# Performance work log

Hardware: AMD Instinct MI355X
Metric: run time of the kernel (lower is better)

The kernel has to match this reference:

```python
import jax, jax.numpy as jnp
import numpy as np

N_VOCAB = 50000
V_SUPPORT = 20000
D = 300
H = 512
B = 8192


def setup_inputs() -> dict:
    key = jax.random.key(0)
    ks = jax.random.split(key, 8)
    ws = jax.random.randint(ks[0], (B,), 0, N_VOCAB, dtype=jnp.int64 if jax.config.jax_enable_x64 else jnp.int32)
    cs = jax.random.randint(ks[1], (B,), 0, N_VOCAB, dtype=ws.dtype)
    vectors = jax.random.normal(ks[2], (N_VOCAB, D), dtype=jnp.float32)
    W1 = jax.random.normal(ks[3], (D, H), dtype=jnp.float32) * (1.0 / np.sqrt(D))
    b1 = jnp.zeros((H,), dtype=jnp.float32)
    W2 = jax.random.normal(ks[4], (H, V_SUPPORT), dtype=jnp.float32) * (1.0 / np.sqrt(H))
    b2 = jnp.zeros((V_SUPPORT,), dtype=jnp.float32)
    vector_to_support = jax.random.randint(ks[5], (N_VOCAB,), 0, V_SUPPORT, dtype=ws.dtype)
    return {"ws": ws, "cs": cs, "vectors": vectors, "W1": W1, "b1": b1,
            "W2": W2, "b2": b2, "vector_to_support": vector_to_support}


def reference(ws, cs, vectors, W1, b1, W2, b2, vector_to_support):
    # embedding lookup of context vectors: [B, D]
    v_c = vectors[cs]
    # FeedForward: Linear -> ReLU -> Linear, then LogSoftmax over support
    h = jax.nn.relu(v_c @ W1 + b1)            # [B, H]
    logits = h @ W2 + b2                       # [B, V]
    logp = jax.nn.log_softmax(logits, axis=-1) # [B, V]
    # map target word (vocab index) -> support index, gather per-row logprob.
    # Original does outputs.T[idx].diag() (O(B^2)); the fused equivalent is a
    # per-row gather: logp[arange(B), idx].
    w_sup = vector_to_support[ws]              # [B]
    logprobs = jnp.take_along_axis(logp, w_sup[:, None], axis=-1)[:, 0]
    return -logprobs                            # [B] NLL per example
```

## Files before the change

kernel.cpp:

```cpp
#include <hip/hip_runtime.h>
#include <hip/hip_bf16.h>
#include <hip/hip_fp8.h>
#include <math.h>


typedef __bf16 bf16x8 __attribute__((ext_vector_type(8)));
typedef float f32x4 __attribute__((ext_vector_type(4)));
typedef int i32x4 __attribute__((ext_vector_type(4)));
typedef int i32x8 __attribute__((ext_vector_type(8)));

#define B_N 8192
#define D_N 300
#define K1K 320
#define H_N 512
#define V_N 20000
#define V_PAD 20480
#define NSPLIT 16
#define SPLIT_V 1280
#define NCH 40
#define ROWS_BLK 128
#define CHUNK_BYTES 16384

#define OFF_PART (8388608u)
#define OFF_W1T  (OFF_PART + 16u*8192u*8u)
#define OFF_B2L  (OFF_W1T + 512u*320u*2u)
#define OFF_H8   (OFF_B2L + 20480u*4u)
#define OFF_W2T8 (OFF_H8 + 8192u*512u)

#define SCALE1 0x7F7F7F7F
#define LOG2E  1.4426950408889634f

__device__ inline unsigned short f2bf(float f) {
  __hip_bfloat16 h = __float2bfloat16(f);
  return *reinterpret_cast<unsigned short*>(&h);
}

__device__ inline unsigned char f2fp8(float f) {
  __hip_fp8_e4m3 q(f);
  return (unsigned char)q.__x;
}

__device__ inline unsigned int pk4_fp8(float a, float b, float c, float d) {
#if __has_builtin(__builtin_amdgcn_cvt_pk_fp8_f32)
  int v = 0;
  v = __builtin_amdgcn_cvt_pk_fp8_f32(a, b, v, false);
  v = __builtin_amdgcn_cvt_pk_fp8_f32(c, d, v, true);
  return (unsigned int)v;
#else
  return (unsigned int)f2fp8(a) | ((unsigned int)f2fp8(b) << 8) |
         ((unsigned int)f2fp8(c) << 16) | ((unsigned int)f2fp8(d) << 24);
#endif
}

__device__ inline float fp82f(unsigned char b) {
  __hip_fp8_e4m3 q; q.__x = b;
  return (float)q;
}

__device__ __forceinline__ void gl16(const void* g, void* l) {
  __builtin_amdgcn_global_load_lds(
      (const __attribute__((address_space(1))) void*)g,
      (__attribute__((address_space(3))) void*)l, 16, 0, 0);
}

__global__ __launch_bounds__(256) void kprep_a(
    const float* __restrict__ W1, unsigned int* __restrict__ W1Tu,
    const float* __restrict__ b2, float* __restrict__ b2l)
{
  __shared__ float tile[64][65];
  const int bid = blockIdx.x;
  const int tid = threadIdx.x;
  if (bid < 40) {
    const int n0 = (bid & 7) * 64;
    const int k0 = (bid >> 3) * 64;
    #pragma unroll
    for (int it = 0; it < 16; ++it) {
      int idx = it * 256 + tid;
      int i = idx >> 6;
      int j = idx & 63;
      float v = 0.f;
      if (k0 + i < D_N) v = W1[(size_t)(k0 + i) * H_N + n0 + j];
      tile[i][j] = v;
    }
    __syncthreads();
    #pragma unroll
    for (int it = 0; it < 8; ++it) {
      int idx = it * 256 + tid;
      int nl = idx >> 5;
      int k = (idx & 31) * 2;
      unsigned int lo = f2bf(tile[k][nl]);
      unsigned int hi = f2bf(tile[k + 1][nl]);
      W1Tu[((size_t)(n0 + nl) * K1K + k0 + k) >> 1] = (hi << 16) | lo;
    }
  } else {
    int i = (bid - 40) * 256 + tid;
    if (i < V_PAD) b2l[i] = (i < V_N) ? b2[i] * LOG2E : -3.0e37f;
  }
}

__global__ __launch_bounds__(256) void kprep_b(
    const int* __restrict__ cs, const float* __restrict__ vectors,
    const unsigned short* __restrict__ W1T, const float* __restrict__ b1,
    unsigned char* __restrict__ h8Out,
    const float* __restrict__ W2, unsigned long long* __restrict__ W2T8u)
{
  __shared__ float tile[64][65];
  __shared__ __align__(16) unsigned short vca[16][328];
  __shared__ int rowIdx[16];
  const int bid = blockIdx.x;
  const int tid = threadIdx.x;

  if (bid >= 512) {
    const int wb = bid - 512;
    const int n0 = (wb >> 3) * 64;
    const int k0 = (wb & 7) * 64;
    #pragma unroll
    for (int it = 0; it < 4; ++it) {
      int idx = it * 256 + tid;
      int i = idx >> 4;
      int j4 = (idx & 15) * 4;
      const float* src = &W2[(size_t)(k0 + i) * V_N + n0 + j4];
      float4 v = make_float4(0.f, 0.f, 0.f, 0.f);
      if (n0 + j4 + 3 < V_N) {
        v = *(const float4*)src;
      } else {
        if (n0 + j4 + 0 < V_N) v.x = src[0];
        if (n0 + j4 + 1 < V_N) v.y = src[1];
        if (n0 + j4 + 2 < V_N) v.z = src[2];
        if (n0 + j4 + 3 < V_N) v.w = src[3];
      }
      tile[i][j4 + 0] = v.x; tile[i][j4 + 1] = v.y;
      tile[i][j4 + 2] = v.z; tile[i][j4 + 3] = v.w;
    }
    __syncthreads();
    #pragma unroll
    for (int it = 0; it < 2; ++it) {
      int idx = it * 256 + tid;
      int nl = idx >> 3;
      int g8 = (idx & 7) * 8;
      int n = n0 + nl;
      unsigned int lo = pk4_fp8(tile[g8 + 0][nl], tile[g8 + 1][nl],
                                tile[g8 + 2][nl], tile[g8 + 3][nl]);
      unsigned int hi = pk4_fp8(tile[g8 + 4][nl], tile[g8 + 5][nl],
                                tile[g8 + 6][nl], tile[g8 + 7][nl]);
      unsigned long long pack = ((unsigned long long)hi << 32) | lo;
      unsigned kk = (unsigned)(k0 + g8);
      unsigned off = ((unsigned)n * 512u + (kk ^ (((unsigned)n & 15u) << 4)));
      W2T8u[off >> 3] = pack;
    }
    return;
  }

  const int lane = tid & 63;
  const int w = tid >> 6;
  const int l15 = lane & 15;
  const int l4 = lane >> 4;
  const int r0 = bid * 16;
  if (tid < 16) rowIdx[tid] = cs[r0 + tid];
  __syncthreads();
  for (int task = tid; task < 16 * 82; task += 256) {
    const int r = task & 15;
    const int g = task >> 4;
    const int k = g * 4;
    float4 v = make_float4(0.f, 0.f, 0.f, 0.f);
    if (k + 3 < D_N)
      v = *(const float4*)(vectors + (size_t)rowIdx[r] * D_N + k);
    ushort4 pk;
    pk.x = f2bf(v.x); pk.y = f2bf(v.y); pk.z = f2bf(v.z); pk.w = f2bf(v.w);
    *(ushort4*)&vca[r][k] = pk;
  }
  __syncthreads();

  bf16x8 afr[10];
  #pragma unroll
  for (int t = 0; t < 10; ++t)
    afr[t] = *(const bf16x8*)&vca[l15][t * 32 + l4 * 8];

  f32x4 acc[8];
  #pragma unroll
  for (int ct = 0; ct < 8; ++ct) acc[ct] = (f32x4){0.f, 0.f, 0.f, 0.f};

  #pragma unroll
  for (int t = 0; t < 10; ++t) {
    #pragma unroll
    for (int ct = 0; ct < 8; ++ct) {
      const int n = w * 128 + ct * 16 + l15;
      bf16x8 bfr = *(const bf16x8*)(W1T + (size_t)n * K1K + t * 32 + l4 * 8);
      acc[ct] = __builtin_amdgcn_mfma_f32_16x16x32_bf16(afr[t], bfr, acc[ct], 0, 0, 0);
    }
  }

  #pragma unroll
  for (int ct = 0; ct < 8; ++ct) {
    const int n = w * 128 + ct * 16 + l15;
    const float bb = b1[n];
    #pragma unroll
    for (int r = 0; r < 4; ++r) {
      const int row = r0 + l4 * 4 + r;
      h8Out[(size_t)row * H_N + n] = f2fp8(fmaxf(acc[ct][r] + bb, 0.f));
    }
  }
}

__device__ __forceinline__ void stage_chunk(const char* g, char* l, int tid) {
  #pragma unroll
  for (int it = 0; it < 4; ++it) {
    const unsigned o = (unsigned)tid * 16 + it * 4096;
    gl16(g + o, l + o);
  }
}

__global__ __launch_bounds__(256, 4) void k3_fused(
    const unsigned char* __restrict__ h8,
    const char* __restrict__ W2T8,
    const float* __restrict__ b2l,
    float2* __restrict__ partOut)
{
  __shared__ __align__(16) char smB[2 * CHUNK_BYTES];
  __shared__ float b2s[SPLIT_V];
  const int tid = threadIdx.x;
  const int lane = tid & 63;
  const int w = tid >> 6;
  const int l15 = lane & 15;
  const int l4 = lane >> 4;
  const int s = blockIdx.x & 15;
  const int rb = blockIdx.x >> 4;
  const int r0 = rb * ROWS_BLK + w * 32;
  const char* gsplit = W2T8 + (size_t)s * SPLIT_V * 512;
  const int sCol = s * SPLIT_V;
  const int c0 = (rb * 7 + s * 3) % NCH;

  i32x8 afr[2][4];
  #pragma unroll
  for (int m = 0; m < 2; ++m) {
    const unsigned char* ap = h8 + (size_t)(r0 + m * 16 + l15) * H_N + l4 * 32;
    #pragma unroll
    for (int t = 0; t < 4; ++t) {
      i32x4 lo = *(const i32x4*)(ap + t * 128);
      i32x4 hi = *(const i32x4*)(ap + t * 128 + 16);
      afr[m][t] = __builtin_shufflevector(lo, hi, 0, 1, 2, 3, 4, 5, 6, 7);
    }
  }

  float s_run[8];
  #pragma unroll
  for (int ri = 0; ri < 8; ++ri) s_run[ri] = 0.f;

  for (int i = tid; i < SPLIT_V; i += 256) b2s[i] = b2l[sCol + i];

  stage_chunk(gsplit + (size_t)c0 * CHUNK_BYTES, smB, tid);

  const unsigned swz = (unsigned)l15 << 4;

  #pragma unroll 1
  for (int i = 0; i < NCH; ++i) {
    const int cc = (c0 + i >= NCH) ? (c0 + i - NCH) : (c0 + i);
    asm volatile("s_waitcnt vmcnt(0) lgkmcnt(0)" ::: "memory");
    __builtin_amdgcn_s_barrier();

    char* cur = smB + (i & 1) * CHUNK_BYTES;
    if (i + 1 < NCH) {
      const int cn = (cc + 1 >= NCH) ? 0 : (cc + 1);
      stage_chunk(gsplit + (size_t)cn * CHUNK_BYTES,
                  smB + ((i & 1) ^ 1) * CHUNK_BYTES, tid);
    }

    const float b2c0 = b2s[cc * 32 + l15];
    const float b2c1 = b2s[cc * 32 + 16 + l15];

    f32x4 acc[2][2];
    #pragma unroll
    for (int m = 0; m < 2; ++m)
      #pragma unroll
      for (int ct = 0; ct < 2; ++ct) acc[m][ct] = (f32x4){0.f, 0.f, 0.f, 0.f};

    #pragma unroll
    for (int t = 0; t < 4; ++t) {
      const char* bp = cur + l15 * 512;
      i32x4 lo = *(const i32x4*)(bp + (((unsigned)(t * 128 + l4 * 32)) ^ swz));
      i32x4 hi = *(const i32x4*)(bp + (((unsigned)(t * 128 + l4 * 32 + 16)) ^ swz));
      i32x8 bfr = __builtin_shufflevector(lo, hi, 0, 1, 2, 3, 4, 5, 6, 7);
      __builtin_amdgcn_s_setprio(1);
      acc[0][0] = __builtin_amdgcn_mfma_scale_f32_16x16x128_f8f6f4(
          afr[0][t], bfr, acc[0][0], 0, 0, 0, SCALE1, 0, SCALE1);
      acc[1][0] = __builtin_amdgcn_mfma_scale_f32_16x16x128_f8f6f4(
          afr[1][t], bfr, acc[1][0], 0, 0, 0, SCALE1, 0, SCALE1);
      __builtin_amdgcn_s_setprio(0);
    }

    #pragma unroll
    for (int t = 0; t < 4; ++t) {
      const char* bp = cur + (16 + l15) * 512;
      i32x4 lo = *(const i32x4*)(bp + (((unsigned)(t * 128 + l4 * 32)) ^ swz));
      i32x4 hi = *(const i32x4*)(bp + (((unsigned)(t * 128 + l4 * 32 + 16)) ^ swz));
      i32x8 bfr = __builtin_shufflevector(lo, hi, 0, 1, 2, 3, 4, 5, 6, 7);
      __builtin_amdgcn_s_setprio(1);
      acc[0][1] = __builtin_amdgcn_mfma_scale_f32_16x16x128_f8f6f4(
          afr[0][t], bfr, acc[0][1], 0, 0, 0, SCALE1, 0, SCALE1);
      acc[1][1] = __builtin_amdgcn_mfma_scale_f32_16x16x128_f8f6f4(
          afr[1][t], bfr, acc[1][1], 0, 0, 0, SCALE1, 0, SCALE1);
      __builtin_amdgcn_s_setprio(0);
      #pragma unroll
      for (int r2 = 0; r2 < 2; ++r2) {
        const int ri = t * 2 + r2;
        const int m_ = ri >> 2, r_ = ri & 3;
        s_run[ri] += __builtin_amdgcn_exp2f(fmaf(acc[m_][0][r_], LOG2E, b2c0));
      }
    }

    #pragma unroll
    for (int m = 0; m < 2; ++m)
      #pragma unroll
      for (int r = 0; r < 4; ++r)
        s_run[m * 4 + r] += __builtin_amdgcn_exp2f(fmaf(acc[m][1][r], LOG2E, b2c1));
  }

  #pragma unroll
  for (int m = 0; m < 2; ++m)
    #pragma unroll
    for (int r = 0; r < 4; ++r) {
      int ri = m * 4 + r;
      float sc = s_run[ri];
      #pragma unroll
      for (int k = 1; k < 16; k <<= 1) sc += __shfl_xor(sc, k);
      if (l15 == 0) {
        int grow = r0 + m * 16 + l4 * 4 + r;
        partOut[(size_t)s * B_N + grow] = make_float2(0.f, sc);
      }
    }
}

__global__ __launch_bounds__(256) void k45_final(
    const unsigned char* __restrict__ h8, const char* __restrict__ W2T8,
    const float* __restrict__ b2, const int* __restrict__ wsIdx,
    const int* __restrict__ v2s, const float2* __restrict__ part,
    float* __restrict__ out)
{
  const int row = blockIdx.x * 4 + (threadIdx.x >> 6);
  const int lane = threadIdx.x & 63;
  const int tc = v2s[wsIdx[row]];
  unsigned long long hv = *(const unsigned long long*)(h8 + (size_t)row * H_N + lane * 8);
  const unsigned off = ((unsigned)(lane * 8)) ^ (((unsigned)tc & 15u) << 4);
  unsigned long long wv = *(const unsigned long long*)(W2T8 + (size_t)tc * 512 + off);
  float sdot = 0.f;
  #pragma unroll
  for (int j = 0; j < 8; ++j)
    sdot += fp82f((unsigned char)(hv >> (8 * j))) * fp82f((unsigned char)(wv >> (8 * j)));
  #pragma unroll
  for (int k = 32; k >= 1; k >>= 1) sdot += __shfl_xor(sdot, k);
  if (lane == 0) {
    const float tgt = sdot + b2[tc];
    float S = 0.f;
    #pragma unroll
    for (int s = 0; s < NSPLIT; ++s) S += part[(size_t)s * B_N + row].y;
    out[row] = logf(S) - tgt;
  }
}

extern "C" void kernel_launch(void* const* d_in, const int* in_sizes, int n_in,
                              void* d_out, int out_size, void* d_ws, size_t ws_size,
                              hipStream_t stream) {
  const int*   wsIdx   = (const int*)d_in[0];
  const int*   cs      = (const int*)d_in[1];
  const float* vectors = (const float*)d_in[2];
  const float* W1      = (const float*)d_in[3];
  const float* b1      = (const float*)d_in[4];
  const float* W2      = (const float*)d_in[5];
  const float* b2      = (const float*)d_in[6];
  const int*   v2s     = (const int*)d_in[7];

  char* wsb = (char*)d_ws;
  float2* part = (float2*)(wsb + OFF_PART);
  unsigned short* W1T = (unsigned short*)(wsb + OFF_W1T);
  float*  b2l  = (float*)(wsb + OFF_B2L);
  unsigned char* h8   = (unsigned char*)(wsb + OFF_H8);
  char*   W2T8 = wsb + OFF_W2T8;
  float*  out  = (float*)d_out;

  hipLaunchKernelGGL(kprep_a, dim3(120), dim3(256), 0, stream,
                     W1, (unsigned int*)W1T, b2, b2l);
  hipLaunchKernelGGL(kprep_b, dim3(512 + 2560), dim3(256), 0, stream,
                     cs, vectors, W1T, b1, h8, W2, (unsigned long long*)W2T8);
  hipLaunchKernelGGL(k3_fused, dim3((B_N / ROWS_BLK) * NSPLIT), dim3(256), 0, stream,
                     h8, W2T8, b2l, part);
  hipLaunchKernelGGL(k45_final, dim3(B_N / 4), dim3(256), 0, stream,
                     h8, W2T8, b2, wsIdx, v2s, part, out);
}
```

Measured before the change: 116.8 us.

## Compute target logit inside main kernel and shrink final reduction kernel

Moves the per-row target-logit dot product out of the final kernel and into 256 extra blocks prepended to the fused GEMM/softmax-sum kernel, so that work overlaps with the main computation. The partial sums are now stored row-major as plain floats instead of split-major float2. This lets the final kernel do one thread per row with four vector loads and a log. It trades the final kernel's scattered reads and wave-wide shuffles for extra blocks in the main grid that may delay the GEMM blocks slightly.

```diff
diff --git a/kernel.cpp b/kernel.cpp
--- a/kernel.cpp
+++ b/kernel.cpp
@@ -20,8 +20,10 @@
 #define NCH 40
 #define ROWS_BLK 128
 #define CHUNK_BYTES 16384
+#define TGT_BLKS 256
 
 #define OFF_PART (8388608u)
+#define OFF_TGT  (OFF_PART + 8192u*16u*4u)
 #define OFF_W1T  (OFF_PART + 16u*8192u*8u)
 #define OFF_B2L  (OFF_W1T + 512u*320u*2u)
 #define OFF_H8   (OFF_B2L + 20480u*4u)
@@ -214,17 +216,46 @@
     const unsigned char* __restrict__ h8,
     const char* __restrict__ W2T8,
     const float* __restrict__ b2l,
-    float2* __restrict__ partOut)
+    const float* __restrict__ b2,
+    const int* __restrict__ wsIdx, const int* __restrict__ v2s,
+    float* __restrict__ partOut,
+    float* __restrict__ tgtOut)
 {
   __shared__ __align__(16) char smB[2 * CHUNK_BYTES];
   __shared__ float b2s[SPLIT_V];
   const int tid = threadIdx.x;
+
+  if (blockIdx.x < TGT_BLKS) {
+    const int row = blockIdx.x * 32 + (tid >> 3);
+    const int j = tid & 7;
+    const int tc = v2s[wsIdx[row]];
+    const unsigned swzt = ((unsigned)tc & 15u) << 4;
+    const unsigned char* hp = h8 + (size_t)row * H_N + j * 64;
+    const char* wp = W2T8 + (size_t)tc * 512;
+    float sdot = 0.f;
+    #pragma unroll
+    for (int q = 0; q < 8; ++q) {
+      unsigned long long hv = *(const unsigned long long*)(hp + q * 8);
+      const unsigned k8 = (unsigned)(j * 64 + q * 8);
+      unsigned long long wv = *(const unsigned long long*)(wp + (k8 ^ swzt));
+      #pragma unroll
+      for (int b = 0; b < 8; ++b)
+        sdot += fp82f((unsigned char)(hv >> (8 * b))) *
+                fp82f((unsigned char)(wv >> (8 * b)));
+    }
+    #pragma unroll
+    for (int k = 1; k < 8; k <<= 1) sdot += __shfl_xor(sdot, k);
+    if (j == 0) tgtOut[row] = sdot + b2[tc];
+    return;
+  }
+
+  const int bid = blockIdx.x - TGT_BLKS;
   const int lane = tid & 63;
   const int w = tid >> 6;
   const int l15 = lane & 15;
   const int l4 = lane >> 4;
-  const int s = blockIdx.x & 15;
-  const int rb = blockIdx.x >> 4;
+  const int s = bid & 15;
+  const int rb = bid >> 4;
   const int r0 = rb * ROWS_BLK + w * 32;
   const char* gsplit = W2T8 + (size_t)s * SPLIT_V * 512;
   const int sCol = s * SPLIT_V;
@@ -325,36 +356,21 @@
       for (int k = 1; k < 16; k <<= 1) sc += __shfl_xor(sc, k);
       if (l15 == 0) {
         int grow = r0 + m * 16 + l4 * 4 + r;
-        partOut[(size_t)s * B_N + grow] = make_float2(0.f, sc);
+        partOut[(size_t)grow * NSPLIT + s] = sc;
       }
     }
 }
 
-__global__ __launch_bounds__(256) void k45_final(
-    const unsigned char* __restrict__ h8, const char* __restrict__ W2T8,
-    const float* __restrict__ b2, const int* __restrict__ wsIdx,
-    const int* __restrict__ v2s, const float2* __restrict__ part,
+__global__ __launch_bounds__(256) void k45b_final(
+    const float* __restrict__ part, const float* __restrict__ tgt,
     float* __restrict__ out)
 {
-  const int row = blockIdx.x * 4 + (threadIdx.x >> 6);
-  const int lane = threadIdx.x & 63;
-  const int tc = v2s[wsIdx[row]];
-  unsigned long long hv = *(const unsigned long long*)(h8 + (size_t)row * H_N + lane * 8);
-  const unsigned off = ((unsigned)(lane * 8)) ^ (((unsigned)tc & 15u) << 4);
-  unsigned long long wv = *(const unsigned long long*)(W2T8 + (size_t)tc * 512 + off);
-  float sdot = 0.f;
-  #pragma unroll
-  for (int j = 0; j < 8; ++j)
-    sdot += fp82f((unsigned char)(hv >> (8 * j))) * fp82f((unsigned char)(wv >> (8 * j)));
-  #pragma unroll
-  for (int k = 32; k >= 1; k >>= 1) sdot += __shfl_xor(sdot, k);
-  if (lane == 0) {
-    const float tgt = sdot + b2[tc];
-    float S = 0.f;
-    #pragma unroll
-    for (int s = 0; s < NSPLIT; ++s) S += part[(size_t)s * B_N + row].y;
-    out[row] = logf(S) - tgt;
-  }
+  const int row = blockIdx.x * 256 + threadIdx.x;
+  const f32x4* p = (const f32x4*)(part + (size_t)row * NSPLIT);
+  f32x4 a = p[0], b = p[1], c = p[2], d = p[3];
+  float S = (a[0] + a[1] + a[2] + a[3]) + (b[0] + b[1] + b[2] + b[3]) +
+            (c[0] + c[1] + c[2] + c[3]) + (d[0] + d[1] + d[2] + d[3]);
+  out[row] = logf(S) - tgt[row];
 }
 
 extern "C" void kernel_launch(void* const* d_in, const int* in_sizes, int n_in,
@@ -370,7 +386,8 @@
   const int*   v2s     = (const int*)d_in[7];
 
   char* wsb = (char*)d_ws;
-  float2* part = (float2*)(wsb + OFF_PART);
+  float*  part = (float*)(wsb + OFF_PART);
+  float*  tgt  = (float*)(wsb + OFF_TGT);
   unsigned short* W1T = (unsigned short*)(wsb + OFF_W1T);
   float*  b2l  = (float*)(wsb + OFF_B2L);
   unsigned char* h8   = (unsigned char*)(wsb + OFF_H8);
@@ -381,8 +398,8 @@
                      W1, (unsigned int*)W1T, b2, b2l);
   hipLaunchKernelGGL(kprep_b, dim3(512 + 2560), dim3(256), 0, stream,
                      cs, vectors, W1T, b1, h8, W2, (unsigned long long*)W2T8);
-  hipLaunchKernelGGL(k3_fused, dim3((B_N / ROWS_BLK) * NSPLIT), dim3(256), 0, stream,
-                     h8, W2T8, b2l, part);
-  hipLaunchKernelGGL(k45_final, dim3(B_N / 4), dim3(256), 0, stream,
-                     h8, W2T8, b2, wsIdx, v2s, part, out);
-}
+  hipLaunchKernelGGL(k3_fused, dim3(TGT_BLKS + (B_N / ROWS_BLK) * NSPLIT), dim3(256),
+                     0, stream, h8, W2T8, b2l, b2, wsIdx, v2s, part, tgt);
+  hipLaunchKernelGGL(k45b_final, dim3(B_N / 256), dim3(256), 0, stream,
+                     part, tgt, out);
+}
```

After: 114.7 us (median of 2 runs). About the same (-1.8%).
